# Performance work log

Hardware: AMD Instinct MI355X
Metric: run time of the kernel (lower is better)

The kernel has to match this reference:

```python
import jax, jax.numpy as jnp
import numpy as np

B, D, DEPTH, C = 8192, 2048, 10, 1000
NUM_INNER = 2 ** DEPTH - 1   # 1023
NUM_LEAVES = 2 ** DEPTH      # 1024


def setup_inputs() -> dict:
    key = jax.random.key(0)
    k1, k2, k3, k4 = jax.random.split(key, 4)
    x = jax.random.normal(k1, (B, D), dtype=jnp.float32)
    # scale weights like a typical init so sigmoid isn't fully saturated
    W = jax.random.normal(k2, (D, NUM_INNER), dtype=jnp.float32) * 0.02
    b = jax.random.normal(k3, (NUM_INNER,), dtype=jnp.float32) * 0.02
    leaf_dist = jax.random.normal(k4, (NUM_LEAVES, C), dtype=jnp.float32)
    return {"x": x, "W": W, "b": b, "leaf_dist": leaf_dist}


def reference(x, W, b, leaf_dist):
    # inner node routing probabilities: [B, num_inner]
    decisions = jax.nn.sigmoid(x @ W + b)
    depth = int(np.log2(decisions.shape[1] + 1))
    pp = jnp.ones((x.shape[0], 1), dtype=x.dtype)  # path probs, starts at root
    for d in range(depth):  # small fixed loop over tree depth
        s, e = 2 ** d - 1, 2 ** (d + 1) - 1
        ld = decisions[:, s:e]                      # [B, 2^d]
        pp = jnp.concatenate([pp * ld, pp * (1.0 - ld)], axis=1)  # [B, 2^(d+1)]
        # faithful reproduction of the original's even/odd reordering
        pp = jnp.concatenate([pp[:, ::2], pp[:, 1::2]], axis=1)
    leaf_probs = jax.nn.softmax(leaf_dist, axis=1)  # [num_leaves, C]
    return pp @ leaf_probs                          # [B, C]
```

## Files before the change

### kernel.cpp

```cpp
#include <hip/hip_runtime.h>

typedef __attribute__((ext_vector_type(8))) unsigned short ushort8v;
typedef __attribute__((ext_vector_type(8))) __bf16 bf16x8;
typedef __attribute__((ext_vector_type(4))) float floatx4;

__device__ __forceinline__ unsigned short f2b(float f) {
    unsigned u = __float_as_uint(f);
    unsigned r = u + 0x7fffu + ((u >> 16) & 1u);
    return (unsigned short)(r >> 16);
}
__device__ __forceinline__ float b2f(unsigned short h) {
    return __uint_as_float(((unsigned)h) << 16);
}


__global__ __launch_bounds__(256) void prep_kernel(const float* __restrict__ x,
                                                   unsigned short* __restrict__ A2x,
                                                   const float* __restrict__ W,
                                                   unsigned short* __restrict__ B2w,
                                                   const float* __restrict__ ld_,
                                                   unsigned short* __restrict__ B2p) {
    __shared__ float tile[32 * 33];
    __shared__ float buf[1000];
    __shared__ float red[8];
    const int b = blockIdx.x, t = threadIdx.x;
    if (b < 512) {
        const int mt = b;
        const int wave = t >> 6, kco = (t >> 4) & 3, l16 = t & 15;
        const float* xr0 = x + (size_t)(mt * 16 + l16) * 2048;
#pragma unroll 4
        for (int i = 0; i < 16; i++) {
            const int kc = wave * 64 + i * 4 + kco;
            const float* xr = xr0 + kc * 8;
            float4 v0 = *(const float4*)xr;
            float4 v1 = *(const float4*)(xr + 4);
            ushort8v o;
            o[0] = f2b(v0.x); o[1] = f2b(v0.y); o[2] = f2b(v0.z); o[3] = f2b(v0.w);
            o[4] = f2b(v1.x); o[5] = f2b(v1.y); o[6] = f2b(v1.z); o[7] = f2b(v1.w);
            *(ushort8v*)(A2x + ((size_t)(mt * 256 + kc) * 16 + l16) * 8) = o;
        }
    } else if (b < 2560) {
        const int idx = b - 512;
        const int n0 = (idx & 31) * 32, k0 = (idx >> 5) * 32;
        const int tx = t & 31, ty = t >> 5;
#pragma unroll
        for (int i = 0; i < 4; i++) {
            int k = k0 + ty + i * 8, n = n0 + tx;
            tile[(ty + i * 8) * 33 + tx] = (n < 1023) ? W[(size_t)k * 1023 + n] : 0.f;
        }
        __syncthreads();
#pragma unroll
        for (int i = 0; i < 4; i++) {
            int n = n0 + ty + i * 8, k = k0 + tx;
            size_t off = ((size_t)((n >> 4) * 256 + (k >> 3)) * 16 + (n & 15)) * 8 + (k & 7);
            B2w[off] = f2b(tile[tx * 33 + ty + i * 8]);
        }
    } else {
        const int l0 = b - 2560;
        const float* r = ld_ + (size_t)l0 * 1000;
        float mx = -3.4e38f;
        for (int i = t; i < 1000; i += 256) { float v = r[i]; buf[i] = v; mx = fmaxf(mx, v); }
#pragma unroll
        for (int o = 32; o > 0; o >>= 1) mx = fmaxf(mx, __shfl_down(mx, o));
        if ((t & 63) == 0) red[t >> 6] = mx;
        __syncthreads();
        mx = fmaxf(fmaxf(red[0], red[1]), fmaxf(red[2], red[3]));
        float s = 0.f;
        for (int i = t; i < 1000; i += 256) { float e = __expf(buf[i] - mx); buf[i] = e; s += e; }
#pragma unroll
        for (int o = 32; o > 0; o >>= 1) s += __shfl_down(s, o);
        if ((t & 63) == 0) red[4 + (t >> 6)] = s;
        __syncthreads();
        float inv = 1.f / (red[4] + red[5] + red[6] + red[7]);
        for (int i = t; i < 1024; i += 256) {
            float pv = (i < 1000) ? buf[i] * inv : 0.f;
            size_t off = ((size_t)((i >> 4) * 128 + (l0 >> 3)) * 16 + (i & 15)) * 8 + (l0 & 7);
            B2p[off] = f2b(pv);
        }
    }
}

__global__ __launch_bounds__(256) void pp_kernel(const unsigned short* __restrict__ dec,
                                                 unsigned short* __restrict__ A2p) {
    __shared__ float d[1024];
    __shared__ float pa[1024], pb[1024];
    const int t = threadIdx.x;
    const int rrow = blockIdx.x;
    const unsigned short* row = dec + (size_t)rrow * 1024;
    for (int i = t; i < 1024; i += 256) d[i] = (i < 1023) ? b2f(row[i]) : 0.f;
    if (t == 0) pa[0] = 1.f;
    __syncthreads();
    float* cur = pa; float* nxt = pb;
    for (int dep = 0; dep < 10; dep++) {
        const int half = 1 << dep;
        const int len = half << 1;
        for (int j = t; j < len; j += 256) {
            int tt = j >> dep;
            int s  = j & (half - 1);
            int i2 = 2 * s + tt;
            int u  = i2 >> dep;
            int rr = i2 & (half - 1);
            float dv = d[half - 1 + rr];
            nxt[j] = cur[rr] * (u ? (1.f - dv) : dv);
        }
        __syncthreads();
        float* tmp = cur; cur = nxt; nxt = tmp;
    }
    const int mtb = (rrow >> 4) * 128;
    const int li  = (rrow & 15) * 8;
    for (int i = t; i < 1024; i += 256) {
        size_t off = ((size_t)(mtb + (i >> 3)) * 16) * 8 + li + (i & 7);
        A2p[off] = f2b(cur[i]);
    }
}

template <int EPI>
__global__ __launch_bounds__(256, 4) void gemm_frag(const unsigned short* __restrict__ A2,
                                                    const unsigned short* __restrict__ B2,
                                                    const float* __restrict__ bias,
                                                    unsigned short* __restrict__ obf,
                                                    float* __restrict__ of32,
                                                    int KC, int ldo) {
    const int tid  = threadIdx.x;
    const int lane = tid & 63;
    const int wave = tid >> 6;
    const int wr = wave >> 1, wc = wave & 1;
    const int quad = lane >> 4, l16 = lane & 15;

    const int l   = blockIdx.x;
    const int xcd = l & 7;
    const int j   = l >> 3;
    const int bmt = xcd * 16 + (j & 15);
    const int bnt = j >> 4;

    const int mt0 = bmt * 4 + wr * 2;
    const int nt0 = bnt * 8 + wc * 4;

    const int lofs = (quad * 16 + l16) * 8;
    const unsigned short* a0 = A2 + (size_t)(mt0 + 0) * KC * 128 + lofs;
    const unsigned short* a1 = A2 + (size_t)(mt0 + 1) * KC * 128 + lofs;
    const unsigned short* b0 = B2 + (size_t)(nt0 + 0) * KC * 128 + lofs;
    const unsigned short* b1 = B2 + (size_t)(nt0 + 1) * KC * 128 + lofs;
    const unsigned short* b2 = B2 + (size_t)(nt0 + 2) * KC * 128 + lofs;
    const unsigned short* b3 = B2 + (size_t)(nt0 + 3) * KC * 128 + lofs;

    floatx4 acc[2][4] = {};
    const int NIT = KC >> 2;

#pragma unroll 2
    for (int it = 0; it < NIT; it++) {
        const size_t ko = (size_t)it * 512;
        bf16x8 af0 = __builtin_bit_cast(bf16x8, *(const ushort8v*)(a0 + ko));
        bf16x8 af1 = __builtin_bit_cast(bf16x8, *(const ushort8v*)(a1 + ko));
        bf16x8 bf0 = __builtin_bit_cast(bf16x8, *(const ushort8v*)(b0 + ko));
        bf16x8 bf1 = __builtin_bit_cast(bf16x8, *(const ushort8v*)(b1 + ko));
        bf16x8 bf2 = __builtin_bit_cast(bf16x8, *(const ushort8v*)(b2 + ko));
        bf16x8 bf3 = __builtin_bit_cast(bf16x8, *(const ushort8v*)(b3 + ko));
        acc[0][0] = __builtin_amdgcn_mfma_f32_16x16x32_bf16(af0, bf0, acc[0][0], 0, 0, 0);
        acc[0][1] = __builtin_amdgcn_mfma_f32_16x16x32_bf16(af0, bf1, acc[0][1], 0, 0, 0);
        acc[0][2] = __builtin_amdgcn_mfma_f32_16x16x32_bf16(af0, bf2, acc[0][2], 0, 0, 0);
        acc[0][3] = __builtin_amdgcn_mfma_f32_16x16x32_bf16(af0, bf3, acc[0][3], 0, 0, 0);
        acc[1][0] = __builtin_amdgcn_mfma_f32_16x16x32_bf16(af1, bf0, acc[1][0], 0, 0, 0);
        acc[1][1] = __builtin_amdgcn_mfma_f32_16x16x32_bf16(af1, bf1, acc[1][1], 0, 0, 0);
        acc[1][2] = __builtin_amdgcn_mfma_f32_16x16x32_bf16(af1, bf2, acc[1][2], 0, 0, 0);
        acc[1][3] = __builtin_amdgcn_mfma_f32_16x16x32_bf16(af1, bf3, acc[1][3], 0, 0, 0);
    }

#pragma unroll
    for (int ni = 0; ni < 4; ni++) {
        const int col = (nt0 + ni) * 16 + l16;
        float bb = 0.f;
        if constexpr (EPI == 0) bb = (col < 1023) ? bias[col] : 0.f;
#pragma unroll
        for (int mi = 0; mi < 2; mi++) {
            const int row0 = (mt0 + mi) * 16 + quad * 4;
#pragma unroll
            for (int r = 0; r < 4; r++) {
                float v = acc[mi][ni][r];
                if constexpr (EPI == 0) {
                    float sgm = 1.f / (1.f + __expf(-(v + bb)));
                    obf[(size_t)(row0 + r) * ldo + col] = f2b(sgm);
                } else {
                    if (col < 1000) of32[(size_t)(row0 + r) * ldo + col] = v;
                }
            }
        }
    }
}

extern "C" void kernel_launch(void* const* d_in, const int* in_sizes, int n_in,
                              void* d_out, int out_size, void* d_ws, size_t ws_size,
                              hipStream_t stream) {
    const float* x   = (const float*)d_in[0];
    const float* W   = (const float*)d_in[1];
    const float* b   = (const float*)d_in[2];
    const float* ldd = (const float*)d_in[3];
    float* out = (float*)d_out;

    char* ws = (char*)d_ws;
    unsigned short* A2x = (unsigned short*)(ws);
    unsigned short* A2p = (unsigned short*)(ws);
    unsigned short* B2w = (unsigned short*)(ws + 33554432);
    unsigned short* dec = (unsigned short*)(ws + 37748736);
    unsigned short* B2p = (unsigned short*)(ws + 54525952);

    prep_kernel<<<3584, 256, 0, stream>>>(x, A2x, W, B2w, ldd, B2p);
    gemm_frag<0><<<1024, 256, 0, stream>>>(A2x, B2w, b, dec, nullptr, 256, 1024);
    pp_kernel<<<8192, 256, 0, stream>>>(dec, A2p);
    gemm_frag<1><<<1024, 256, 0, stream>>>(A2p, B2p, nullptr, nullptr, out, 128, 1000);
}
```

Baseline: 226.1 us.

## Enlarge per-wave GEMM register tile to 4x8 MFMA fragments with 2-wave blocks

Each wave now computes a 64x128 output tile (4x8 16x16 fragments) instead of 32x64, and blocks shrink to 2 waves covering 128x128. Each fragment loaded from global memory is reused across more MFMAs, so load traffic per FLOP drops. The cost is 32 accumulator vectors per wave, which means high register pressure and low occupancy (launch bounds 128,1). Only 512 blocks of 2 waves are launched, roughly 1024 waves across the GPU, which can leave latency poorly hidden since there is no LDS staging.

```diff
diff --git a/kernel.cpp b/kernel.cpp
--- a/kernel.cpp
+++ b/kernel.cpp
@@ -115,7 +115,7 @@
 }
 
 template <int EPI>
-__global__ __launch_bounds__(256, 4) void gemm_frag(const unsigned short* __restrict__ A2,
+__global__ __launch_bounds__(128, 1) void gemm_frag(const unsigned short* __restrict__ A2,
                                                     const unsigned short* __restrict__ B2,
                                                     const float* __restrict__ bias,
                                                     unsigned short* __restrict__ obf,
@@ -124,55 +124,53 @@
     const int tid  = threadIdx.x;
     const int lane = tid & 63;
     const int wave = tid >> 6;
-    const int wr = wave >> 1, wc = wave & 1;
     const int quad = lane >> 4, l16 = lane & 15;
 
     const int l   = blockIdx.x;
     const int xcd = l & 7;
     const int j   = l >> 3;
-    const int bmt = xcd * 16 + (j & 15);
-    const int bnt = j >> 4;
-
-    const int mt0 = bmt * 4 + wr * 2;
-    const int nt0 = bnt * 8 + wc * 4;
+    const int bm  = xcd * 8 + (j & 7);
+    const int bn  = j >> 3;
+
+    const int mt0 = bm * 8 + wave * 4;
+    const int nt0 = bn * 8;
 
     const int lofs = (quad * 16 + l16) * 8;
-    const unsigned short* a0 = A2 + (size_t)(mt0 + 0) * KC * 128 + lofs;
-    const unsigned short* a1 = A2 + (size_t)(mt0 + 1) * KC * 128 + lofs;
-    const unsigned short* b0 = B2 + (size_t)(nt0 + 0) * KC * 128 + lofs;
-    const unsigned short* b1 = B2 + (size_t)(nt0 + 1) * KC * 128 + lofs;
-    const unsigned short* b2 = B2 + (size_t)(nt0 + 2) * KC * 128 + lofs;
-    const unsigned short* b3 = B2 + (size_t)(nt0 + 3) * KC * 128 + lofs;
-
-    floatx4 acc[2][4] = {};
+    const unsigned short* ap[4];
+    const unsigned short* bp[8];
+#pragma unroll
+    for (int mi = 0; mi < 4; mi++) ap[mi] = A2 + (size_t)(mt0 + mi) * KC * 128 + lofs;
+#pragma unroll
+    for (int ni = 0; ni < 8; ni++) bp[ni] = B2 + (size_t)(nt0 + ni) * KC * 128 + lofs;
+
+    floatx4 acc[4][8] = {};
     const int NIT = KC >> 2;
 
 #pragma unroll 2
     for (int it = 0; it < NIT; it++) {
         const size_t ko = (size_t)it * 512;
-        bf16x8 af0 = __builtin_bit_cast(bf16x8, *(const ushort8v*)(a0 + ko));
-        bf16x8 af1 = __builtin_bit_cast(bf16x8, *(const ushort8v*)(a1 + ko));
-        bf16x8 bf0 = __builtin_bit_cast(bf16x8, *(const ushort8v*)(b0 + ko));
-        bf16x8 bf1 = __builtin_bit_cast(bf16x8, *(const ushort8v*)(b1 + ko));
-        bf16x8 bf2 = __builtin_bit_cast(bf16x8, *(const ushort8v*)(b2 + ko));
-        bf16x8 bf3 = __builtin_bit_cast(bf16x8, *(const ushort8v*)(b3 + ko));
-        acc[0][0] = __builtin_amdgcn_mfma_f32_16x16x32_bf16(af0, bf0, acc[0][0], 0, 0, 0);
-        acc[0][1] = __builtin_amdgcn_mfma_f32_16x16x32_bf16(af0, bf1, acc[0][1], 0, 0, 0);
-        acc[0][2] = __builtin_amdgcn_mfma_f32_16x16x32_bf16(af0, bf2, acc[0][2], 0, 0, 0);
-        acc[0][3] = __builtin_amdgcn_mfma_f32_16x16x32_bf16(af0, bf3, acc[0][3], 0, 0, 0);
-        acc[1][0] = __builtin_amdgcn_mfma_f32_16x16x32_bf16(af1, bf0, acc[1][0], 0, 0, 0);
-        acc[1][1] = __builtin_amdgcn_mfma_f32_16x16x32_bf16(af1, bf1, acc[1][1], 0, 0, 0);
-        acc[1][2] = __builtin_amdgcn_mfma_f32_16x16x32_bf16(af1, bf2, acc[1][2], 0, 0, 0);
-        acc[1][3] = __builtin_amdgcn_mfma_f32_16x16x32_bf16(af1, bf3, acc[1][3], 0, 0, 0);
-    }
-
-#pragma unroll
-    for (int ni = 0; ni < 4; ni++) {
+        bf16x8 af[4], bfv[8];
+#pragma unroll
+        for (int mi = 0; mi < 4; mi++)
+            af[mi] = __builtin_bit_cast(bf16x8, *(const ushort8v*)(ap[mi] + ko));
+#pragma unroll
+        for (int ni = 0; ni < 8; ni++)
+            bfv[ni] = __builtin_bit_cast(bf16x8, *(const ushort8v*)(bp[ni] + ko));
+#pragma unroll
+        for (int mi = 0; mi < 4; mi++)
+#pragma unroll
+            for (int ni = 0; ni < 8; ni++)
+                acc[mi][ni] = __builtin_amdgcn_mfma_f32_16x16x32_bf16(
+                    af[mi], bfv[ni], acc[mi][ni], 0, 0, 0);
+    }
+
+#pragma unroll
+    for (int ni = 0; ni < 8; ni++) {
         const int col = (nt0 + ni) * 16 + l16;
         float bb = 0.f;
         if constexpr (EPI == 0) bb = (col < 1023) ? bias[col] : 0.f;
 #pragma unroll
-        for (int mi = 0; mi < 2; mi++) {
+        for (int mi = 0; mi < 4; mi++) {
             const int row0 = (mt0 + mi) * 16 + quad * 4;
 #pragma unroll
             for (int r = 0; r < 4; r++) {
@@ -205,7 +203,7 @@
     unsigned short* B2p = (unsigned short*)(ws + 54525952);
 
     prep_kernel<<<3584, 256, 0, stream>>>(x, A2x, W, B2w, ldd, B2p);
-    gemm_frag<0><<<1024, 256, 0, stream>>>(A2x, B2w, b, dec, nullptr, 256, 1024);
+    gemm_frag<0><<<512, 128, 0, stream>>>(A2x, B2w, b, dec, nullptr, 256, 1024);
     pp_kernel<<<8192, 256, 0, stream>>>(dec, A2p);
-    gemm_frag<1><<<1024, 256, 0, stream>>>(A2p, B2p, nullptr, nullptr, out, 128, 1000);
-}
+    gemm_frag<1><<<512, 128, 0, stream>>>(A2p, B2p, nullptr, nullptr, out, 128, 1000);
+}
```

New measurement: 228.5 us. Within noise of the previous version (+1.1%).
